# Performance work log

Hardware: AMD Instinct MI355X
Metric: run time of the kernel (lower is better)

## Reference

```python
import jax, jax.numpy as jnp
import numpy as np

A, I = 16, 16           # n_agents, n_items
D = A * I               # flattened bid dim
ROUNDS = 40             # sinkhorn_rounds
EPS = 0.1               # sinkhorn_epsilon
B = 32768               # batch size


def setup_inputs() -> dict:
    key = jax.random.key(0)
    ks = jax.random.split(key, 20)

    def lin(k, din, dout):
        k1, k2 = jax.random.split(k)
        s = 1.0 / np.sqrt(din)
        W = jax.random.uniform(k1, (din, dout), minval=-s, maxval=s, dtype=jnp.float32)
        b = jax.random.uniform(k2, (dout,), minval=-s, maxval=s, dtype=jnp.float32)
        return W, b

    inp = {"bids": jax.random.uniform(ks[0], (B, A, I), dtype=jnp.float32)}
    dims_a = [(D, 128), (128, 128), (128, 128), (128, D)]
    dims_p = [(D, 128), (128, 128), (128, 128), (128, A)]
    for i, (din, dout) in enumerate(dims_a):
        W, b = lin(ks[1 + i], din, dout)
        inp[f"aw{i}"] = W
        inp[f"ab{i}"] = b
    for i, (din, dout) in enumerate(dims_p):
        W, b = lin(ks[5 + i], din, dout)
        inp[f"pw{i}"] = W
        inp[f"pb{i}"] = b
    return inp


def _log_sinkhorn(log_K, log_a, log_b):
    # log_K: [B, A+1, I+1]; log_a: [A+1]; log_b: [I+1]
    def step(K, _):
        K = K + (log_a - jax.scipy.special.logsumexp(K, axis=-1))[..., :, None]
        K = K + (log_b - jax.scipy.special.logsumexp(K, axis=-2))[..., None, :]
        return K, None
    K, _ = jax.lax.scan(step, log_K, None, length=ROUNDS)
    return jnp.exp(K)


def _forward(bids, aw0, ab0, aw1, ab1, aw2, ab2, aw3, ab3,
             pw0, pb0, pw1, pb1, pw2, pb2, pw3, pb3):
    bsz = bids.shape[0]
    X = bids.reshape(bsz, D)

    h = jnp.tanh(X @ aw0 + ab0)
    h = jnp.tanh(h @ aw1 + ab1)
    h = jnp.tanh(h @ aw2 + ab2)
    augmented = h @ aw3 + ab3                     # [B, A*I]

    # bipartite matching via log-domain Sinkhorn on padded matrix
    mat = augmented.reshape(bsz, A, I)
    padded = -jnp.pad(mat, ((0, 0), (0, 1), (0, 1)))  # [B, A+1, I+1]
    # 'unit' marginals: each agent/item has mass 1, dummies absorb the rest
    log_a = jnp.log(jnp.concatenate([jnp.ones(A, jnp.float32), jnp.full((1,), float(I), jnp.float32)]))
    log_b = jnp.log(jnp.concatenate([jnp.ones(I, jnp.float32), jnp.full((1,), float(A), jnp.float32)]))
    plan = _log_sinkhorn(-padded / EPS, log_a, log_b)
    allocs = plan[:, :A, :I]                      # drop dummy row/col

    p = jnp.tanh(X @ pw0 + pb0)
    p = jnp.tanh(p @ pw1 + pb1)
    p = jnp.tanh(p @ pw2 + pb2)
    frac = jax.nn.sigmoid(p @ pw3 + pb3)          # [B, A]
    payments = frac * (allocs * bids).sum(axis=-1)
    return allocs, payments


def reference(bids, aw0, ab0, aw1, ab1, aw2, ab2, aw3, ab3,
              pw0, pb0, pw1, pb1, pw2, pb2, pw3, pb3):
    return _forward(bids, aw0, ab0, aw1, ab1, aw2, ab2, aw3, ab3,
                    pw0, pb0, pw1, pb1, pw2, pb2, pw3, pb3)
```

## Files before the change

### kernel.cpp

```cpp
#include <hip/hip_runtime.h>

#define NB 32768

typedef _Float16 half8 __attribute__((ext_vector_type(8)));
typedef float floatx4 __attribute__((ext_vector_type(4)));
typedef float floatx2 __attribute__((ext_vector_type(2)));
typedef unsigned int uint4v __attribute__((ext_vector_type(4)));

#define MFMA16(a,b,c) __builtin_amdgcn_mfma_f32_16x16x32_f16(a,b,c,0,0,0)

__device__ __forceinline__ float rcp_f(float x){ return __builtin_amdgcn_rcpf(x); }
__device__ __forceinline__ float exp2_f(float x){ return __builtin_amdgcn_exp2f(x); }
__device__ __forceinline__ float tanh_f(float x){
  float e = exp2_f(x * 2.8853900817779268f);
  return (e - 1.0f) * rcp_f(e + 1.0f);
}
__device__ __forceinline__ float sigmoid_f(float x){
  return rcp_f(1.0f + exp2_f(-1.4426950408889634f * x));
}

__device__ __forceinline__ floatx2 pk_mul2(floatx2 a, floatx2 b){
  floatx2 d; asm("v_pk_mul_f32 %0, %1, %2" : "=v"(d) : "v"(a), "v"(b)); return d;
}
__device__ __forceinline__ floatx2 pk_fma2(floatx2 a, floatx2 b, floatx2 c){
  floatx2 d; asm("v_pk_fma_f32 %0, %1, %2, %3" : "=v"(d) : "v"(a), "v"(b), "v"(c)); return d;
}

template<int CTRL>
__device__ __forceinline__ float dpp_qp(float x){
  return __builtin_bit_cast(float, __builtin_amdgcn_update_dpp(0, __builtin_bit_cast(int,x), CTRL, 0xF, 0xF, true));
}
__device__ __forceinline__ float qadd2(float x){
  x += dpp_qp<0xB1>(x);
  x += dpp_qp<0x4E>(x);
  return x;
}
__device__ __forceinline__ float qmax2(float x){
  x = fmaxf(x, dpp_qp<0xB1>(x));
  x = fmaxf(x, dpp_qp<0x4E>(x));
  return x;
}

constexpr int O_AW0H = 0;
constexpr int O_AW1H = 32768;
constexpr int O_AW2H = 49152;
constexpr int O_AW3H = 65536;
constexpr int O_PW0H = 98304;
constexpr int O_PW1H = 131072;
constexpr int O_PW2H = 147456;
constexpr int O_PW3H = 163840;
constexpr int O_AW1L = 165888;
constexpr int O_AW2L = 182272;
constexpr int O_AW3L = 198656;

struct PrepJob { const float* src; _Float16* h; _Float16* l; int nshift; int total; };
struct PrepJobs { PrepJob j[8]; };

__global__ void prep_kernel(PrepJobs js){
  const PrepJob jb = js.j[blockIdx.y];
  const int idx = blockIdx.x*256 + threadIdx.x;
  if (idx >= jb.total) return;
  const int N = 1 << jb.nshift;
  const int n = idx & (N-1);
  const int k = idx >> jb.nshift;
  const int K = jb.total >> jb.nshift;
  float w = jb.src[idx];
  _Float16 h = (_Float16)w;
  jb.h[(long)n*K + k] = h;
  if (jb.l) jb.l[(long)n*K + k] = (_Float16)(w - (float)h);
}

__device__ __forceinline__ int aaddr(int row, int col){
  int cc = (col >> 2) ^ (row & 7);
  return row*128 + (cc<<2) + (col & 3);
}

template<bool NEED_LO>
__device__ __forceinline__ void read_frag(const unsigned int* __restrict__ act,
    int row, int ks, int q, half8& ah, half8& al)
{
  const int s = row & 7;
  const int cc0 = ks*8 + q*2;
  uint4v c0 = *(const uint4v*)(act + row*128 + (((cc0  ) ^ s)<<2));
  uint4v c1 = *(const uint4v*)(act + row*128 + (((cc0+1) ^ s)<<2));
  uint4v h;
  h.x = (c0.x & 0xffffu) | (c0.y << 16);
  h.y = (c0.z & 0xffffu) | (c0.w << 16);
  h.z = (c1.x & 0xffffu) | (c1.y << 16);
  h.w = (c1.z & 0xffffu) | (c1.w << 16);
  ah = __builtin_bit_cast(half8, h);
  if constexpr (NEED_LO){
    uint4v g;
    g.x = (c0.x >> 16) | (c0.y & 0xffff0000u);
    g.y = (c0.z >> 16) | (c0.w & 0xffff0000u);
    g.z = (c1.x >> 16) | (c1.y & 0xffff0000u);
    g.w = (c1.z >> 16) | (c1.w & 0xffff0000u);
    al = __builtin_bit_cast(half8, g);
  }
}

__device__ __forceinline__ unsigned int pack_act(float v){
  _Float16 h = (_Float16)v;
  _Float16 lo = (_Float16)(v - (float)h);
  return (unsigned int)__builtin_bit_cast(unsigned short, h)
       | ((unsigned int)__builtin_bit_cast(unsigned short, lo) << 16);
}
__device__ __forceinline__ unsigned int pack_act_hi(float v){
  return (unsigned int)__builtin_bit_cast(unsigned short, (_Float16)v);
}

template<int KS, bool LO>
__device__ __forceinline__ void load_tile(
    const _Float16* __restrict__ Wh, const _Float16* __restrict__ Wl,
    int K, int nt, int l15, int q, half8* bh, half8* bl)
{
  const _Float16* bp = Wh + (nt*16 + l15)*K + q*8;
#pragma unroll
  for (int ks=0; ks<KS; ++ks) bh[ks] = *(const half8*)(bp + ks*32);
  if constexpr (LO){
    const _Float16* blp = Wl + (nt*16 + l15)*K + q*8;
#pragma unroll
    for (int ks=0; ks<KS; ++ks) bl[ks] = *(const half8*)(blp + ks*32);
  }
}

template<int KS, int PASSES, int NT, int RING, typename EPI>
__device__ __forceinline__ void mfma_stream4(
    const half8 (&Ah)[4][KS], const half8 (&Al)[4][KS],
    const _Float16* __restrict__ Wh, const _Float16* __restrict__ Wl,
    int K, int nt0, int l15, int q, EPI&& epi)
{
  half8 Bh[RING][KS], Bl[RING][KS];
  load_tile<KS,PASSES==3>(Wh, Wl, K, nt0, l15, q, Bh[0], Bl[0]);
  if constexpr (RING > 2){
    if constexpr (NT > 1)
      load_tile<KS,PASSES==3>(Wh, Wl, K, nt0+1, l15, q, Bh[1], Bl[1]);
  }
#pragma unroll
  for (int nt=0; nt<NT; ++nt){
    constexpr int PD = RING - 1;
    if (nt+PD < NT)
      load_tile<KS,PASSES==3>(Wh, Wl, K, nt0+nt+PD, l15, q, Bh[(nt+PD)%RING], Bl[(nt+PD)%RING]);
    floatx4 acc[4];
#pragma unroll
    for (int m=0; m<4; ++m) acc[m] = (floatx4)0.0f;
#pragma unroll
    for (int ks=0; ks<KS; ++ks){
      const half8 bh = Bh[nt%RING][ks];
#pragma unroll
      for (int m=0; m<4; ++m)
        acc[m] = MFMA16(Ah[m][ks], bh, acc[m]);
      if constexpr (PASSES == 3){
        const half8 bl = Bl[nt%RING][ks];
#pragma unroll
        for (int m=0; m<4; ++m){
          acc[m] = MFMA16(Al[m][ks], bh, acc[m]);
          acc[m] = MFMA16(Ah[m][ks], bl, acc[m]);
        }
      }
    }
    epi(nt0+nt, acc);
  }
}

__global__ __launch_bounds__(256, 2) void fused_kernel(
  const float* __restrict__ X, const _Float16* __restrict__ WT,
  const float* __restrict__ ab0, const float* __restrict__ ab1,
  const float* __restrict__ ab2, const float* __restrict__ ab3,
  const float* __restrict__ pb0, const float* __restrict__ pb1,
  const float* __restrict__ pb2, const float* __restrict__ pb3,
  float* __restrict__ out)
{
  __shared__ unsigned int S[64*256 + 1024];
  unsigned int* act_a = S;
  unsigned int* act_p = S + 8192;
  float* frac_l = (float*)(S + 16384);
  const int t = threadIdx.x;
  const int w = t >> 6;
  const int l = t & 63, q = l>>4, l15 = l&15;
  const int nt0 = w*2;
  const long rb = (long)blockIdx.x * 64;

  auto epi_act = [&](unsigned int* act, const float* bias, bool lo){
    return [=](int ntg, auto& acc){
      float bb = bias[ntg*16 + l15];
#pragma unroll
      for (int m=0; m<4; ++m){
#pragma unroll
        for (int r=0; r<4; ++r){
          float tv = tanh_f(acc[m][r] + bb);
          act[aaddr(m*16 + q*4 + r, ntg*16 + l15)] = lo ? pack_act(tv) : pack_act_hi(tv);
        }
      }
    };
  };

  {
    half8 Xf[4][8];
#pragma unroll
    for (int mt=0; mt<4; ++mt){
      float4 xa[8], xb[8];
#pragma unroll
      for (int ks=0; ks<8; ++ks){
        const float* xp = X + (rb + mt*16 + l15)*256 + ks*32 + q*8;
        xa[ks] = *(const float4*)(xp);
        xb[ks] = *(const float4*)(xp + 4);
      }
#pragma unroll
      for (int ks=0; ks<8; ++ks){
        half8 h;
        h[0]=(_Float16)xa[ks].x; h[1]=(_Float16)xa[ks].y; h[2]=(_Float16)xa[ks].z; h[3]=(_Float16)xa[ks].w;
        h[4]=(_Float16)xb[ks].x; h[5]=(_Float16)xb[ks].y; h[6]=(_Float16)xb[ks].z; h[7]=(_Float16)xb[ks].w;
        Xf[mt][ks] = h;
      }
    }
    mfma_stream4<8,1,2,2>(Xf, Xf, WT+O_AW0H, WT+O_AW0H, 256, nt0, l15, q,
                          epi_act(act_a, ab0, true));
    mfma_stream4<8,1,2,2>(Xf, Xf, WT+O_PW0H, WT+O_PW0H, 256, nt0, l15, q,
                          epi_act(act_p, pb0, false));
  }
  __syncthreads();

#pragma unroll 1
  for (int st=0; st<2; ++st){
    const _Float16* Wah = WT + (st ? O_AW2H : O_AW1H);
    const _Float16* Wal = WT + (st ? O_AW2L : O_AW1L);
    const _Float16* Wph = WT + (st ? O_PW2H : O_PW1H);
    const float* ba = st ? ab2 : ab1;
    const float* bp = st ? pb2 : pb1;
    {
      half8 Fah[4][4], Fal[4][4];
#pragma unroll
      for (int m=0; m<4; ++m)
#pragma unroll
        for (int ks=0; ks<4; ++ks)
          read_frag<true>(act_a, m*16 + l15, ks, q, Fah[m][ks], Fal[m][ks]);
      __syncthreads();
      mfma_stream4<4,3,2,2>(Fah, Fal, Wah, Wal, 128, nt0, l15, q,
                            epi_act(act_a, ba, true));
    }
    {
      half8 Fph[4][4], du;
#pragma unroll
      for (int m=0; m<4; ++m)
#pragma unroll
        for (int ks=0; ks<4; ++ks)
          read_frag<false>(act_p, m*16 + l15, ks, q, Fph[m][ks], du);
      __syncthreads();
      mfma_stream4<4,1,2,3>(Fph, Fph, Wph, Wph, 128, nt0, l15, q,
                            epi_act(act_p, bp, false));
    }
    __syncthreads();
  }

  {
    half8 Fah[4][4], Fal[4][4], Fph[4][4], du;
#pragma unroll
    for (int m=0; m<4; ++m)
#pragma unroll
      for (int ks=0; ks<4; ++ks)
        read_frag<true>(act_a, m*16 + l15, ks, q, Fah[m][ks], Fal[m][ks]);
    if (w == 0){
#pragma unroll
      for (int m=0; m<4; ++m)
#pragma unroll
        for (int ks=0; ks<4; ++ks)
          read_frag<false>(act_p, m*16 + l15, ks, q, Fph[m][ks], du);
    }
    __syncthreads();
    if (w == 0){
      mfma_stream4<4,1,1,2>(Fph, Fph, WT+O_PW3H, WT+O_PW3H, 128, 0, l15, q,
        [&](int, auto& acc){
          float bb = pb3[l15];
#pragma unroll
          for (int m=0; m<4; ++m)
#pragma unroll
            for (int r=0; r<4; ++r)
              frac_l[(m*16 + q*4 + r)*16 + l15] = sigmoid_f(acc[m][r] + bb);
        });
    }
    float* augl = (float*)S;
    const int ncol0 = w*64;
    mfma_stream4<4,3,4,2>(Fah, Fal,
                          WT+O_AW3H + ncol0*128, WT+O_AW3L + ncol0*128,
                          128, 0, l15, q,
      [&](int nt, auto& acc){
        float bb = ab3[ncol0 + nt*16 + l15];
#pragma unroll
        for (int m=0; m<4; ++m)
#pragma unroll
          for (int r=0; r<4; ++r)
            augl[(m*16 + q*4 + r)*256 + ncol0 + nt*16 + l15] = acc[m][r] + bb;
      });
    __syncthreads();
  }

  const int c = l & 3;
  const float Ssc = 14.426950408889634f;
  const float cmask = (c == 3) ? 1.0f : 0.0f;
  const int eL = w*16 + (l >> 2);
  const long e = rb + eL;

  floatx2 Kp[4][8];
  floatx2 KPp[8];

  const float* ap = (const float*)S + eL*256 + 4*c;
#pragma unroll
  for (int k=0;k<8;++k){
    float4 va = *(const float4*)(ap + (2*k  )*16);
    float4 vb = *(const float4*)(ap + (2*k+1)*16);
    Kp[0][k] = (floatx2){va.x*Ssc, vb.x*Ssc};
    Kp[1][k] = (floatx2){va.y*Ssc, vb.y*Ssc};
    Kp[2][k] = (floatx2){va.z*Ssc, vb.z*Ssc};
    Kp[3][k] = (floatx2){va.w*Ssc, vb.w*Ssc};
  }

#pragma unroll
  for (int k=0;k<8;++k){
    float m0 = fmaxf(fmaxf(Kp[0][k].x,Kp[1][k].x), fmaxf(Kp[2][k].x,Kp[3][k].x));
    m0 = qmax2(fmaxf(m0, 0.0f));
    float m1 = fmaxf(fmaxf(Kp[0][k].y,Kp[1][k].y), fmaxf(Kp[2][k].y,Kp[3][k].y));
    m1 = qmax2(fmaxf(m1, 0.0f));
    Kp[0][k] = (floatx2){exp2_f(Kp[0][k].x-m0), exp2_f(Kp[0][k].y-m1)};
    Kp[1][k] = (floatx2){exp2_f(Kp[1][k].x-m0), exp2_f(Kp[1][k].y-m1)};
    Kp[2][k] = (floatx2){exp2_f(Kp[2][k].x-m0), exp2_f(Kp[2][k].y-m1)};
    Kp[3][k] = (floatx2){exp2_f(Kp[3][k].x-m0), exp2_f(Kp[3][k].y-m1)};
    KPp[k]   = (floatx2){cmask*exp2_f(-m0), cmask*exp2_f(-m1)};
  }

  float vj0=1.f, vj1=1.f, vj2=1.f, vj3=1.f;
  float v16 = cmask;
  floatx2 u2[8];
  float u16;

  for (int r=0;r<40;++r){
    floatx2 b0=(floatx2){vj0,vj0}, b1=(floatx2){vj1,vj1};
    floatx2 b2=(floatx2){vj2,vj2}, b3=(floatx2){vj3,vj3};
    floatx2 b16=(floatx2){v16,v16};
#pragma unroll
    for (int k=0;k<8;++k){
      floatx2 pp = pk_mul2(Kp[0][k], b0);
      pp = pk_fma2(Kp[1][k], b1, pp);
      pp = pk_fma2(Kp[2][k], b2, pp);
      pp = pk_fma2(Kp[3][k], b3, pp);
      pp = pk_fma2(KPp[k], b16, pp);
      float px = qadd2(pp.x);
      float py = qadd2(pp.y);
      u2[k] = (floatx2){rcp_f(px), rcp_f(py)};
    }
    {
      float p16 = (vj0+vj1) + (vj2+vj3) + cmask*v16;
      p16 = qadd2(p16);
      u16 = 16.0f * rcp_f(p16);
    }
    floatx2 t0p = pk_mul2(Kp[0][0], u2[0]);
    floatx2 t1p = pk_mul2(Kp[1][0], u2[0]);
    floatx2 t2p = pk_mul2(Kp[2][0], u2[0]);
    floatx2 t3p = pk_mul2(Kp[3][0], u2[0]);
    floatx2 tPp = pk_mul2(KPp[0],   u2[0]);
#pragma unroll
    for (int k=1;k<8;++k){
      t0p = pk_fma2(Kp[0][k], u2[k], t0p);
      t1p = pk_fma2(Kp[1][k], u2[k], t1p);
      t2p = pk_fma2(Kp[2][k], u2[k], t2p);
      t3p = pk_fma2(Kp[3][k], u2[k], t3p);
      tPp = pk_fma2(KPp[k],   u2[k], tPp);
    }
    float t0 = t0p.x + t0p.y + u16;
    float t1 = t1p.x + t1p.y + u16;
    float t2 = t2p.x + t2p.y + u16;
    float t3 = t3p.x + t3p.y + u16;
    float t16 = tPp.x + tPp.y + cmask*u16;
    vj0 = rcp_f(t0); vj1 = rcp_f(t1); vj2 = rcp_f(t2); vj3 = rcp_f(t3);
    v16 = cmask * 16.0f * rcp_f(t16 + 1e-30f + (1.0f - cmask));
  }

  float* op = out + e*256 + 4*c;
  const float* bpx = X + e*256 + 4*c;
  float pv0=0.f, pv1=0.f, pv2=0.f, pv3=0.f;
#pragma unroll
  for (int k=0;k<8;++k){
#pragma unroll
    for (int h=0;h<2;++h){
      const int i = 2*k + h;
      const float uu = h ? u2[k].y : u2[k].x;
      const float K0 = h ? Kp[0][k].y : Kp[0][k].x;
      const float K1 = h ? Kp[1][k].y : Kp[1][k].x;
      const float K2 = h ? Kp[2][k].y : Kp[2][k].x;
      const float K3 = h ? Kp[3][k].y : Kp[3][k].x;
      float4 wv;
      wv.x = uu*K0*vj0;
      wv.y = uu*K1*vj1;
      wv.z = uu*K2*vj2;
      wv.w = uu*K3*vj3;
      *(float4*)(op + i*16) = wv;
      float4 bb = *(const float4*)(bpx + i*16);
      float s = wv.x*bb.x + wv.y*bb.y + wv.z*bb.z + wv.w*bb.w;
      s = qadd2(s);
      if ((i>>2) == c){
        const int rr = i & 3;
        if      (rr==0) pv0 = s;
        else if (rr==1) pv1 = s;
        else if (rr==2) pv2 = s;
        else            pv3 = s;
      }
    }
  }
  const float4 fr = *(const float4*)(frac_l + eL*16 + 4*c);
  float4 pvv;
  pvv.x = pv0*fr.x; pvv.y = pv1*fr.y; pvv.z = pv2*fr.z; pvv.w = pv3*fr.w;
  *(float4*)(out + (size_t)NB*256 + e*16 + 4*c) = pvv;
}

extern "C" void kernel_launch(void* const* d_in, const int* in_sizes, int n_in,
                              void* d_out, int out_size, void* d_ws, size_t ws_size,
                              hipStream_t stream)
{
  const float* bids = (const float*)d_in[0];
  const float* aw0 = (const float*)d_in[1];  const float* ab0 = (const float*)d_in[2];
  const float* aw1 = (const float*)d_in[3];  const float* ab1 = (const float*)d_in[4];
  const float* aw2 = (const float*)d_in[5];  const float* ab2 = (const float*)d_in[6];
  const float* aw3 = (const float*)d_in[7];  const float* ab3 = (const float*)d_in[8];
  const float* pw0 = (const float*)d_in[9];  const float* pb0 = (const float*)d_in[10];
  const float* pw1 = (const float*)d_in[11]; const float* pb1 = (const float*)d_in[12];
  const float* pw2 = (const float*)d_in[13]; const float* pb2 = (const float*)d_in[14];
  const float* pw3 = (const float*)d_in[15]; const float* pb3 = (const float*)d_in[16];

  _Float16* WT = (_Float16*)d_ws;

  PrepJobs js;
  js.j[0] = { aw0, WT+O_AW0H, nullptr,    7, 32768 };
  js.j[1] = { aw1, WT+O_AW1H, WT+O_AW1L,  7, 16384 };
  js.j[2] = { aw2, WT+O_AW2H, WT+O_AW2L,  7, 16384 };
  js.j[3] = { aw3, WT+O_AW3H, WT+O_AW3L,  8, 32768 };
  js.j[4] = { pw0, WT+O_PW0H, nullptr,    7, 32768 };
  js.j[5] = { pw1, WT+O_PW1H, nullptr,    7, 16384 };
  js.j[6] = { pw2, WT+O_PW2H, nullptr,    7, 16384 };
  js.j[7] = { pw3, WT+O_PW3H, nullptr,    4, 2048  };

  prep_kernel<<<dim3(128,8), 256, 0, stream>>>(js);
  fused_kernel<<<dim3(NB/64), 256, 0, stream>>>(bids, WT, ab0,ab1,ab2,ab3,
                                                pb0,pb1,pb2,pb3, (float*)d_out);
}
```

Measured before the change: 184.9 us.

## Tile weight transpose through LDS and pad augmented-logit smem stride

The weight prep kernel now transposes through a padded 64x65 shared tile, so both the global reads and the global writes are coalesced instead of scattered strided stores. Separately, the fused kernel's shared buffer for the augmented logits uses a row stride of 260 floats instead of 256, meant to avoid LDS bank conflicts when the Sinkhorn stage reads rows as float4. Shared memory grows slightly, and frac_l moves to make room.

```diff
diff --git a/kernel.cpp b/kernel.cpp
--- a/kernel.cpp
+++ b/kernel.cpp
@@ -53,21 +53,42 @@
 constexpr int O_AW2L = 182272;
 constexpr int O_AW3L = 198656;
 
-struct PrepJob { const float* src; _Float16* h; _Float16* l; int nshift; int total; };
+struct PrepJob { const float* src; _Float16* h; _Float16* l; int K; int N; };
 struct PrepJobs { PrepJob j[8]; };
 
-__global__ void prep_kernel(PrepJobs js){
+__global__ __launch_bounds__(256) void prep_kernel(PrepJobs js){
   const PrepJob jb = js.j[blockIdx.y];
-  const int idx = blockIdx.x*256 + threadIdx.x;
-  if (idx >= jb.total) return;
-  const int N = 1 << jb.nshift;
-  const int n = idx & (N-1);
-  const int k = idx >> jb.nshift;
-  const int K = jb.total >> jb.nshift;
-  float w = jb.src[idx];
-  _Float16 h = (_Float16)w;
-  jb.h[(long)n*K + k] = h;
-  if (jb.l) jb.l[(long)n*K + k] = (_Float16)(w - (float)h);
+  const int tiles_n = (jb.N + 63) >> 6;
+  const int tk = blockIdx.x / tiles_n;
+  const int tn = blockIdx.x % tiles_n;
+  if (tk * 64 >= jb.K) return;
+
+  __shared__ unsigned int T[64][65];
+  const int lane = threadIdx.x & 63;
+  const int row4 = threadIdx.x >> 6;
+
+#pragma unroll 4
+  for (int r = row4; r < 64; r += 4){
+    const int k = tk*64 + r, n = tn*64 + lane;
+    if (k < jb.K && n < jb.N){
+      float w = jb.src[(long)k*jb.N + n];
+      _Float16 h = (_Float16)w;
+      _Float16 lo = (_Float16)(w - (float)h);
+      T[r][lane] = (unsigned int)__builtin_bit_cast(unsigned short, h)
+                 | ((unsigned int)__builtin_bit_cast(unsigned short, lo) << 16);
+    }
+  }
+  __syncthreads();
+#pragma unroll 4
+  for (int r = row4; r < 64; r += 4){
+    const int n = tn*64 + r, k = tk*64 + lane;
+    if (n < jb.N && k < jb.K){
+      unsigned int p = T[lane][r];
+      jb.h[(long)n*jb.K + k] = __builtin_bit_cast(_Float16, (unsigned short)(p & 0xffffu));
+      if (jb.l)
+        jb.l[(long)n*jb.K + k] = __builtin_bit_cast(_Float16, (unsigned short)(p >> 16));
+    }
+  }
 }
 
 __device__ __forceinline__ int aaddr(int row, int col){
@@ -171,10 +192,11 @@
   const float* __restrict__ pb2, const float* __restrict__ pb3,
   float* __restrict__ out)
 {
-  __shared__ unsigned int S[64*256 + 1024];
+  __shared__ unsigned int S[17664];
   unsigned int* act_a = S;
   unsigned int* act_p = S + 8192;
-  float* frac_l = (float*)(S + 16384);
+  float* frac_l = (float*)(S + 16640);
+  constexpr int AUGS = 260;
   const int t = threadIdx.x;
   const int w = t >> 6;
   const int l = t & 63, q = l>>4, l15 = l&15;
@@ -290,7 +312,7 @@
         for (int m=0; m<4; ++m)
 #pragma unroll
           for (int r=0; r<4; ++r)
-            augl[(m*16 + q*4 + r)*256 + ncol0 + nt*16 + l15] = acc[m][r] + bb;
+            augl[(m*16 + q*4 + r)*AUGS + ncol0 + nt*16 + l15] = acc[m][r] + bb;
       });
     __syncthreads();
   }
@@ -304,7 +326,7 @@
   floatx2 Kp[4][8];
   floatx2 KPp[8];
 
-  const float* ap = (const float*)S + eL*256 + 4*c;
+  const float* ap = (const float*)S + eL*AUGS + 4*c;
 #pragma unroll
   for (int k=0;k<8;++k){
     float4 va = *(const float4*)(ap + (2*k  )*16);
@@ -429,16 +451,16 @@
   _Float16* WT = (_Float16*)d_ws;
 
   PrepJobs js;
-  js.j[0] = { aw0, WT+O_AW0H, nullptr,    7, 32768 };
-  js.j[1] = { aw1, WT+O_AW1H, WT+O_AW1L,  7, 16384 };
-  js.j[2] = { aw2, WT+O_AW2H, WT+O_AW2L,  7, 16384 };
-  js.j[3] = { aw3, WT+O_AW3H, WT+O_AW3L,  8, 32768 };
-  js.j[4] = { pw0, WT+O_PW0H, nullptr,    7, 32768 };
-  js.j[5] = { pw1, WT+O_PW1H, nullptr,    7, 16384 };
-  js.j[6] = { pw2, WT+O_PW2H, nullptr,    7, 16384 };
-  js.j[7] = { pw3, WT+O_PW3H, nullptr,    4, 2048  };
-
-  prep_kernel<<<dim3(128,8), 256, 0, stream>>>(js);
+  js.j[0] = { aw0, WT+O_AW0H, nullptr,   256, 128 };
+  js.j[1] = { aw1, WT+O_AW1H, WT+O_AW1L, 128, 128 };
+  js.j[2] = { aw2, WT+O_AW2H, WT+O_AW2L, 128, 128 };
+  js.j[3] = { aw3, WT+O_AW3H, WT+O_AW3L, 128, 256 };
+  js.j[4] = { pw0, WT+O_PW0H, nullptr,   256, 128 };
+  js.j[5] = { pw1, WT+O_PW1H, nullptr,   128, 128 };
+  js.j[6] = { pw2, WT+O_PW2H, nullptr,   128, 128 };
+  js.j[7] = { pw3, WT+O_PW3H, nullptr,   128,  16 };
+
+  prep_kernel<<<dim3(8,8), 256, 0, stream>>>(js);
   fused_kernel<<<dim3(NB/64), 256, 0, stream>>>(bids, WT, ab0,ab1,ab2,ab3,
                                                 pb0,pb1,pb2,pb3, (float*)d_out);
 }
```

After: 186.5 us. Within noise of the previous version (+0.9%).
